# Optimization experiments

Measured on AMD Instinct MI355X. Metric: run time of the kernel, lower is better.

## Reference

```python
import jax, jax.numpy as jnp
import numpy as np

D = 128  # node_dim (hardcoded in the torch module)


def _bn(x, g, b, eps=1e-5):
    # BatchNorm1d in training mode: per-batch mean / biased variance
    m = x.mean(0)
    v = x.var(0)
    return (x - m) * jax.lax.rsqrt(v + eps) * g + b


def setup_inputs() -> dict:
    key = jax.random.key(0)
    ks = jax.random.split(key, 16)
    N, E, ED = 4096, 16384, 16
    node = jax.random.normal(ks[0], (N, D), jnp.float32)
    edge = jax.random.normal(ks[1], (E, ED), jnp.float32)
    hidden = jax.random.normal(ks[2], (1, N, D), jnp.float32)
    edge_index = jax.random.randint(ks[3], (E, 2), 0, N)

    def lin(k, o, i):
        return jax.random.normal(k, (o, i), jnp.float32) / np.sqrt(i).astype(np.float32)

    W1 = lin(ks[4], 256, ED)
    W2 = lin(ks[5], 256, 256)
    W3 = lin(ks[6], 128, 256)
    W4 = lin(ks[7], D * D, 128)
    g1, b1 = jnp.ones(256), jnp.zeros(256)
    g2, b2 = jnp.ones(256), jnp.zeros(256)
    g3, b3 = jnp.ones(128), jnp.zeros(128)
    g4, b4 = jnp.ones(D * D), jnp.zeros(D * D)
    lim = 1.0 / np.sqrt(D).astype(np.float32)
    bias = jax.random.uniform(ks[8], (D,), jnp.float32, -lim, lim)
    W_ih = lin(ks[9], 3 * D, D)
    W_hh = lin(ks[10], 3 * D, D)
    b_ih = jnp.zeros(3 * D)
    b_hh = jnp.zeros(3 * D)
    return dict(node=node, edge_index=edge_index, edge=edge, hidden=hidden,
                W1=W1, g1=g1, b1=b1, W2=W2, g2=g2, b2=b2, W3=W3, g3=g3, b3=b3,
                W4=W4, g4=g4, b4=b4, bias=bias, W_ih=W_ih, W_hh=W_hh,
                b_ih=b_ih, b_hh=b_hh)


def reference(node, edge_index, edge, hidden, W1, g1, b1, W2, g2, b2,
              W3, g3, b3, W4, g4, b4, bias, W_ih, W_hh, b_ih, b_hh):
    N = node.shape[0]
    E = edge.shape[0]
    h0 = hidden[0]  # [N, D]
    src, dst = edge_index[:, 0], edge_index[:, 1]

    # edge encoder -> per-edge [D, D] weight matrix
    x = jax.nn.relu(_bn(edge @ W1.T, g1, b1))
    x = jax.nn.relu(_bn(x @ W2.T, g2, b2))
    x = jax.nn.relu(_bn(x @ W3.T, g3, b3))
    w = _bn(x @ W4.T, g4, b4).reshape(E, D, D)

    # gather source nodes, per-edge vector-matrix product
    x_i = node[src]                               # [E, D]
    msg = jnp.einsum('ed,edk->ek', x_i, w)        # [E, D]

    # scatter-mean over destination nodes
    sums = jax.ops.segment_sum(msg, dst, num_segments=N)
    cnt = jax.ops.segment_sum(jnp.ones((E, 1), msg.dtype), dst, num_segments=N)
    message = sums / jnp.maximum(cnt, 1.0)
    m = jax.nn.relu(message + bias)               # [N, D]

    # single-step GRU (PyTorch gate order r, z, n)
    gi = m @ W_ih.T + b_ih
    gh = h0 @ W_hh.T + b_hh
    r = jax.nn.sigmoid(gi[:, :D] + gh[:, :D])
    z = jax.nn.sigmoid(gi[:, D:2 * D] + gh[:, D:2 * D])
    n = jnp.tanh(gi[:, 2 * D:] + r * gh[:, 2 * D:])
    hn = (1.0 - z) * n + z * h0                   # [N, D]
    return hn, hn[None]
```

## Files before the change

### kernel.cpp

```cpp
#include <hip/hip_runtime.h>

#define EPS 1e-5f

typedef _Float16 half8 __attribute__((ext_vector_type(8)));
typedef _Float16 half4 __attribute__((ext_vector_type(4)));
typedef float f32x16 __attribute__((ext_vector_type(16)));

__global__ __launch_bounds__(256) void gemm_abt(const float* __restrict__ A,
                                                const float* __restrict__ B,
                                                _Float16* __restrict__ C,
                                                int M, int N, int K,
                                                float* __restrict__ osum,
                                                float* __restrict__ osq) {
  __shared__ float As[16][68];
  __shared__ float Bs[16][68];
  const int t = threadIdx.x;
  const int tx = t & 15, ty = t >> 4;
  const int m0 = blockIdx.y * 64, n0 = blockIdx.x * 64;
  float acc[4][4] = {};
  for (int k0 = 0; k0 < K; k0 += 16) {
    __syncthreads();
    {
      const int r = t >> 2;
      const int kk = (t & 3) << 2;
      float4 av = *(const float4*)&A[(size_t)(m0 + r) * K + k0 + kk];
      As[kk + 0][r] = av.x; As[kk + 1][r] = av.y;
      As[kk + 2][r] = av.z; As[kk + 3][r] = av.w;
      float4 bv = *(const float4*)&B[(size_t)(n0 + r) * K + k0 + kk];
      Bs[kk + 0][r] = bv.x; Bs[kk + 1][r] = bv.y;
      Bs[kk + 2][r] = bv.z; Bs[kk + 3][r] = bv.w;
    }
    __syncthreads();
#pragma unroll
    for (int kk = 0; kk < 16; ++kk) {
      float4 a = *(const float4*)&As[kk][ty << 2];
      float4 b = *(const float4*)&Bs[kk][tx << 2];
      float av[4] = {a.x, a.y, a.z, a.w};
      float bv[4] = {b.x, b.y, b.z, b.w};
#pragma unroll
      for (int i = 0; i < 4; ++i)
#pragma unroll
        for (int j = 0; j < 4; ++j) acc[i][j] += av[i] * bv[j];
    }
  }
#pragma unroll
  for (int i = 0; i < 4; ++i) {
    half4 o;
    o[0] = (_Float16)acc[i][0]; o[1] = (_Float16)acc[i][1];
    o[2] = (_Float16)acc[i][2]; o[3] = (_Float16)acc[i][3];
    *(half4*)&C[(size_t)(m0 + (ty << 2) + i) * N + n0 + (tx << 2)] = o;
  }
  __syncthreads();
  float* sred = (float*)As;
  if (t < 128) sred[t] = 0.f;
  __syncthreads();
#pragma unroll
  for (int j = 0; j < 4; ++j) {
    float s = 0.f, sq = 0.f;
#pragma unroll
    for (int i = 0; i < 4; ++i) {
      float v = acc[i][j];
      s += v; sq += v * v;
    }
    atomicAdd(&sred[((tx << 2) + j) * 2 + 0], s);
    atomicAdd(&sred[((tx << 2) + j) * 2 + 1], sq);
  }
  __syncthreads();
  if (t < 64) {
    atomicAdd(&osum[n0 + t], sred[t * 2]);
    atomicAdd(&osq[n0 + t], sred[t * 2 + 1]);
  }
}

template <int TRANS, bool STATS, bool AH, bool CH>
__global__ __launch_bounds__(256) void gemm16(const void* __restrict__ Ap,
                                              const float* __restrict__ B,
                                              void* __restrict__ Cp,
                                              int lda, int ldb, int ldc, int K,
                                              const float* __restrict__ s1,
                                              const float* __restrict__ s2,
                                              const float* __restrict__ g,
                                              const float* __restrict__ b,
                                              float invM,
                                              float* __restrict__ osum,
                                              float* __restrict__ osq) {
  __shared__ _Float16 As[128 * 64];
  __shared__ _Float16 Bs[128 * 64];
  __shared__ float scL[256], shL[256];
  const int t = threadIdx.x;
  const int m0 = blockIdx.y * 128, n0 = blockIdx.x * 128;
  const int w = t >> 6, l = t & 63;
  const int wm = w >> 1, wn = w & 1;
  const int lr = l & 31, lg = l >> 5;
  if (TRANS == 1) {
    if (t < K) {
      float mean = s1[t] * invM;
      float var = s2[t] * invM - mean * mean;
      float sc = g[t] * rsqrtf(var + EPS);
      scL[t] = sc;
      shL[t] = b[t] - mean * sc;
    }
  }
  f32x16 acc[2][2];
#pragma unroll
  for (int i = 0; i < 2; ++i)
#pragma unroll
    for (int j = 0; j < 2; ++j) acc[i][j] = (f32x16){0.f};
  for (int k0 = 0; k0 < K; k0 += 64) {
    __syncthreads();
#pragma unroll
    for (int i = 0; i < 4; ++i) {
      const int gq = i * 256 + t;
      const int f = gq >> 6, lp = gq & 63;
      const int row = (f >> 2) * 32 + (lp & 31);
      const int c = (f & 3) * 16 + (lp >> 5) * 8;
      float va[8];
      if (AH) {
        const _Float16* ap = (const _Float16*)Ap + (size_t)(m0 + row) * lda + k0 + c;
        half8 av = *(const half8*)ap;
#pragma unroll
        for (int j = 0; j < 8; ++j) va[j] = (float)av[j];
      } else {
        const float* ap = (const float*)Ap + (size_t)(m0 + row) * lda + k0 + c;
        float4 a4 = *(const float4*)ap, b4 = *(const float4*)(ap + 4);
        va[0] = a4.x; va[1] = a4.y; va[2] = a4.z; va[3] = a4.w;
        va[4] = b4.x; va[5] = b4.y; va[6] = b4.z; va[7] = b4.w;
      }
      if (TRANS == 1) {
#pragma unroll
        for (int j = 0; j < 8; ++j)
          va[j] = fmaxf(va[j] * scL[k0 + c + j] + shL[k0 + c + j], 0.f);
      }
      half8 h;
#pragma unroll
      for (int j = 0; j < 8; ++j) h[j] = (_Float16)va[j];
      *(half8*)(As + (size_t)gq * 8) = h;
      const float* bp = B + (size_t)(n0 + row) * ldb + k0 + c;
      float4 e4 = *(const float4*)bp, f4 = *(const float4*)(bp + 4);
      half8 hb;
      hb[0] = (_Float16)e4.x; hb[1] = (_Float16)e4.y; hb[2] = (_Float16)e4.z; hb[3] = (_Float16)e4.w;
      hb[4] = (_Float16)f4.x; hb[5] = (_Float16)f4.y; hb[6] = (_Float16)f4.z; hb[7] = (_Float16)f4.w;
      *(half8*)(Bs + (size_t)gq * 8) = hb;
    }
    __syncthreads();
#pragma unroll
    for (int ks = 0; ks < 4; ++ks) {
      half8 af[2], bf[2];
#pragma unroll
      for (int mb = 0; mb < 2; ++mb) {
        af[mb] = *(const half8*)(As + (size_t)(((wm * 2 + mb) * 4 + ks) * 64 + l) * 8);
        bf[mb] = *(const half8*)(Bs + (size_t)(((wn * 2 + mb) * 4 + ks) * 64 + l) * 8);
      }
#pragma unroll
      for (int mb = 0; mb < 2; ++mb)
#pragma unroll
        for (int nb = 0; nb < 2; ++nb)
          acc[mb][nb] = __builtin_amdgcn_mfma_f32_32x32x16_f16(af[mb], bf[nb], acc[mb][nb], 0, 0, 0);
    }
  }
#pragma unroll
  for (int mb = 0; mb < 2; ++mb)
#pragma unroll
    for (int nb = 0; nb < 2; ++nb)
#pragma unroll
      for (int r = 0; r < 16; ++r) {
        const int row = m0 + wm * 64 + mb * 32 + (r & 3) + 8 * (r >> 2) + 4 * lg;
        const int col = n0 + wn * 64 + nb * 32 + lr;
        if (CH) ((_Float16*)Cp)[(size_t)row * ldc + col] = (_Float16)acc[mb][nb][r];
        else ((float*)Cp)[(size_t)row * ldc + col] = acc[mb][nb][r];
      }
  if (STATS) {
    __syncthreads();
    float* sred = (float*)As;
    if (t < 256) sred[t] = 0.f;
    __syncthreads();
#pragma unroll
    for (int nb = 0; nb < 2; ++nb) {
      float s = 0.f, sq = 0.f;
#pragma unroll
      for (int mb = 0; mb < 2; ++mb)
#pragma unroll
        for (int r = 0; r < 16; ++r) {
          float v = acc[mb][nb][r];
          s += v; sq += v * v;
        }
      const int cl = wn * 64 + nb * 32 + lr;
      atomicAdd(&sred[cl * 2 + 0], s);
      atomicAdd(&sred[cl * 2 + 1], sq);
    }
    __syncthreads();
    if (t < 128) {
      atomicAdd(&osum[n0 + t], sred[t * 2]);
      atomicAdd(&osq[n0 + t], sred[t * 2 + 1]);
    }
  }
}

__global__ __launch_bounds__(256) void gram_kernel(const _Float16* __restrict__ y3,
                                                   float* __restrict__ part,
                                                   const float* __restrict__ s3sum,
                                                   const float* __restrict__ s3sq,
                                                   const float* __restrict__ g3,
                                                   const float* __restrict__ b3,
                                                   float invE,
                                                   float* __restrict__ colsum) {
  __shared__ float xL[128 * 132];
  __shared__ float scL[128], shL[128];
  const int t = threadIdx.x, tx = t & 15, ty = t >> 4;
  if (t < 128) {
    float mean = s3sum[t] * invE;
    float var = s3sq[t] * invE - mean * mean;
    float sc = g3[t] * rsqrtf(var + EPS);
    scL[t] = sc;
    shL[t] = b3[t] - mean * sc;
  }
  __syncthreads();
  const int r0 = blockIdx.x * 128;
#pragma unroll
  for (int i = 0; i < 16; ++i) {
    int f4 = t + i * 256;
    int r = f4 >> 5;
    int c4 = (f4 & 31) << 2;
    half4 hv = *(const half4*)&y3[(size_t)(r0 + r) * 128 + c4];
    float4 v;
    v.x = fmaxf((float)hv[0] * scL[c4 + 0] + shL[c4 + 0], 0.f);
    v.y = fmaxf((float)hv[1] * scL[c4 + 1] + shL[c4 + 1], 0.f);
    v.z = fmaxf((float)hv[2] * scL[c4 + 2] + shL[c4 + 2], 0.f);
    v.w = fmaxf((float)hv[3] * scL[c4 + 3] + shL[c4 + 3], 0.f);
    *(float4*)&xL[r * 132 + c4] = v;
  }
  __syncthreads();
  float acc[8][8] = {};
  float csum[8] = {};
  for (int r = 0; r < 128; ++r) {
    float4 a0 = *(const float4*)&xL[r * 132 + ty * 8];
    float4 a1 = *(const float4*)&xL[r * 132 + ty * 8 + 4];
    float4 b0 = *(const float4*)&xL[r * 132 + tx * 8];
    float4 b1 = *(const float4*)&xL[r * 132 + tx * 8 + 4];
    float a[8] = {a0.x, a0.y, a0.z, a0.w, a1.x, a1.y, a1.z, a1.w};
    float b[8] = {b0.x, b0.y, b0.z, b0.w, b1.x, b1.y, b1.z, b1.w};
#pragma unroll
    for (int i = 0; i < 8; ++i)
#pragma unroll
      for (int j = 0; j < 8; ++j) acc[i][j] += a[i] * b[j];
    if (tx == ty) {
#pragma unroll
      for (int i = 0; i < 8; ++i) csum[i] += a[i];
    }
  }
  float* base = part + (size_t)blockIdx.x * 16384;
#pragma unroll
  for (int i = 0; i < 8; ++i)
#pragma unroll
    for (int j = 0; j < 8; ++j)
      base[(ty * 8 + i) * 128 + tx * 8 + j] = acc[i][j];
  if (tx == ty) {
#pragma unroll
    for (int i = 0; i < 8; ++i) atomicAdd(&colsum[ty * 8 + i], csum[i]);
  }
}

__global__ __launch_bounds__(256) void gram_reduce(const float* __restrict__ part,
                                                   float* __restrict__ out) {
  int idx = blockIdx.x * 256 + threadIdx.x;
  float s = 0.f;
  for (int b = 0; b < 128; ++b) s += part[(size_t)b * 16384 + idx];
  out[idx] = s;
}

__global__ __launch_bounds__(256) void w4_finalize(const float* __restrict__ W4,
                                                   const float* __restrict__ U,
                                                   const float* __restrict__ colsum3,
                                                   const float* __restrict__ g4,
                                                   const float* __restrict__ b4,
                                                   _Float16* __restrict__ BTf,
                                                   float* __restrict__ t4,
                                                   float invM) {
  const int r = (blockIdx.x * 256 + threadIdx.x) >> 6;
  const int lane = threadIdx.x & 63;
  const float* wp = W4 + (size_t)r * 128;
  const float* up = U + (size_t)r * 128;
  float p1 = 0.f, p2 = 0.f;
#pragma unroll
  for (int c0 = 0; c0 < 128; c0 += 64) {
    float wv = wp[c0 + lane];
    p1 += up[c0 + lane] * wv;
    p2 += colsum3[c0 + lane] * wv;
  }
#pragma unroll
  for (int off = 32; off > 0; off >>= 1) {
    p1 += __shfl_down(p1, off);
    p2 += __shfl_down(p2, off);
  }
  p1 = __shfl(p1, 0);
  p2 = __shfl(p2, 0);
  float m4 = p2 * invM;
  float q = p1 * invM;
  float s = g4[r] * rsqrtf(q - m4 * m4 + EPS);
  if (lane == 0) t4[r] = b4[r] - m4 * s;
  const int kout = r & 127, d = r >> 7;
  if (lane < 16) {
    const int ks = lane >> 1, lg = lane & 1;
    const float* cp = wp + lane * 8;
    float4 va = *(const float4*)cp, vb = *(const float4*)(cp + 4);
    half8 h;
    h[0] = (_Float16)(s * va.x); h[1] = (_Float16)(s * va.y);
    h[2] = (_Float16)(s * va.z); h[3] = (_Float16)(s * va.w);
    h[4] = (_Float16)(s * vb.x); h[5] = (_Float16)(s * vb.y);
    h[6] = (_Float16)(s * vb.z); h[7] = (_Float16)(s * vb.w);
    size_t off16 = (size_t)d * 16384 +
                   (size_t)((((kout >> 5) * 8 + ks) * 64) + (kout & 31) + lg * 32) * 8;
    *(half8*)(BTf + off16) = h;
  }
}

__global__ __launch_bounds__(256, 2) void zgemm(const _Float16* __restrict__ y3,
                                                const float* __restrict__ node,
                                                const int* __restrict__ eidx,
                                                const _Float16* __restrict__ BTf,
                                                const float* __restrict__ Tn,
                                                const float* __restrict__ s3sum,
                                                const float* __restrict__ s3sq,
                                                const float* __restrict__ g3,
                                                const float* __restrict__ b3,
                                                float invE,
                                                float* __restrict__ sums) {
  __shared__ __align__(16) _Float16 Bs[2][16384];
  __shared__ _Float16 xiL[32 * 128];
  __shared__ float scL[128], shL[128];
  const int t = threadIdx.x;
  const int e0 = blockIdx.y * 128;
  const int d0 = blockIdx.x * 32;
  const int w = t >> 6, l = t & 63;
  const int wm = w >> 1, wn = w & 1;
  const int lr = l & 31, lg = l >> 5;
  if (t < 128) {
    float mean = s3sum[t] * invE;
    float var = s3sq[t] * invE - mean * mean;
    float sc = g3[t] * rsqrtf(var + EPS);
    scL[t] = sc;
    shL[t] = b3[t] - mean * sc;
  }
  {
    const int e = t >> 1, db = (t & 1) * 16;
    const int src = eidx[(e0 + e) * 2];
    const float* np = node + (size_t)src * 128 + d0 + db;
#pragma unroll
    for (int j = 0; j < 16; j += 4) {
      float4 v = *(const float4*)(np + j);
      xiL[(db + j + 0) * 128 + e] = (_Float16)v.x;
      xiL[(db + j + 1) * 128 + e] = (_Float16)v.y;
      xiL[(db + j + 2) * 128 + e] = (_Float16)v.z;
      xiL[(db + j + 3) * 128 + e] = (_Float16)v.w;
    }
  }
  half8 st[8];
  {
    const _Float16* p = BTf + (size_t)d0 * 16384 + (size_t)t * 8;
#pragma unroll
    for (int j = 0; j < 8; ++j) st[j] = *(const half8*)(p + j * 2048);
  }
#pragma unroll
  for (int j = 0; j < 8; ++j) *(half8*)(&Bs[0][0] + t * 8 + j * 2048) = st[j];
  {
    const _Float16* p = BTf + (size_t)(d0 + 1) * 16384 + (size_t)t * 8;
#pragma unroll
    for (int j = 0; j < 8; ++j) st[j] = *(const half8*)(p + j * 2048);
  }
  __syncthreads();
  half8 xf[2][8];
#pragma unroll
  for (int mb = 0; mb < 2; ++mb) {
    const _Float16* xp = y3 + (size_t)(e0 + wm * 64 + mb * 32 + lr) * 128 + lg * 8;
#pragma unroll
    for (int ks = 0; ks < 8; ++ks) {
      const int c = ks * 16 + lg * 8;
      half8 hv = *(const half8*)(xp + ks * 16);
      half8 h;
#pragma unroll
      for (int j = 0; j < 8; ++j)
        h[j] = (_Float16)fmaxf((float)hv[j] * scL[c + j] + shL[c + j], 0.f);
      xf[mb][ks] = h;
    }
  }
  f32x16 acc00 = (f32x16){0.f}, acc01 = (f32x16){0.f};
  f32x16 acc10 = (f32x16){0.f}, acc11 = (f32x16){0.f};

  for (int dt = 0; dt < 32; ++dt) {
    const _Float16* bs = &Bs[dt & 1][0];
    _Float16* bsn = &Bs[(dt + 1) & 1][0];
    const _Float16 xv0 = xiL[dt * 128 + wm * 64 + lr];
    const _Float16 xv1 = xiL[dt * 128 + wm * 64 + 32 + lr];
    const half8 xb0 = {xv0, xv0, xv0, xv0, xv0, xv0, xv0, xv0};
    const half8 xb1 = {xv1, xv1, xv1, xv1, xv1, xv1, xv1, xv1};
    __builtin_amdgcn_s_setprio(1);
#pragma unroll
    for (int ks = 0; ks < 8; ++ks) {
      half8 b0 = *(const half8*)(bs + (size_t)(((wn * 2 + 0) * 8 + ks) * 64 + l) * 8);
      half8 b1 = *(const half8*)(bs + (size_t)(((wn * 2 + 1) * 8 + ks) * 64 + l) * 8);
      if (dt < 31) *(half8*)(bsn + t * 8 + ks * 2048) = st[ks];
      half8 a0 = xf[0][ks] * xb0;
      half8 a1 = xf[1][ks] * xb1;
      acc00 = __builtin_amdgcn_mfma_f32_32x32x16_f16(a0, b0, acc00, 0, 0, 0);
      acc01 = __builtin_amdgcn_mfma_f32_32x32x16_f16(a0, b1, acc01, 0, 0, 0);
      acc10 = __builtin_amdgcn_mfma_f32_32x32x16_f16(a1, b0, acc10, 0, 0, 0);
      acc11 = __builtin_amdgcn_mfma_f32_32x32x16_f16(a1, b1, acc11, 0, 0, 0);
    }
    __builtin_amdgcn_s_setprio(0);
    if (dt < 30) {
      const _Float16* p = BTf + (size_t)(d0 + dt + 2) * 16384 + (size_t)t * 8;
#pragma unroll
      for (int j = 0; j < 8; ++j) st[j] = *(const half8*)(p + j * 2048);
    }
    asm volatile("s_waitcnt lgkmcnt(0)" ::: "memory");
    __builtin_amdgcn_s_barrier();
  }
  const bool add_t = (blockIdx.x == 0);
#pragma unroll
  for (int r = 0; r < 16; ++r) {
    const int rl = (r & 3) + 8 * (r >> 2) + 4 * lg;
    const int eA = e0 + wm * 64 + rl;
    const int eB = eA + 32;
    const int dA = eidx[eA * 2 + 1], sA = eidx[eA * 2];
    const int dB = eidx[eB * 2 + 1], sB = eidx[eB * 2];
    const int c0 = wn * 64 + lr;
    float v00 = acc00[r], v01 = acc01[r], v10 = acc10[r], v11 = acc11[r];
    if (add_t) {
      v00 += Tn[(size_t)sA * 128 + c0];
      v01 += Tn[(size_t)sA * 128 + c0 + 32];
      v10 += Tn[(size_t)sB * 128 + c0];
      v11 += Tn[(size_t)sB * 128 + c0 + 32];
    }
    atomicAdd(&sums[(size_t)dA * 128 + c0], v00);
    atomicAdd(&sums[(size_t)dA * 128 + c0 + 32], v01);
    atomicAdd(&sums[(size_t)dB * 128 + c0], v10);
    atomicAdd(&sums[(size_t)dB * 128 + c0 + 32], v11);
  }
}

__global__ __launch_bounds__(128) void t4n_kernel(const float* __restrict__ node,
                                                  const float* __restrict__ t4,
                                                  float* __restrict__ Tn,
                                                  const int* __restrict__ eidx,
                                                  float* __restrict__ cnt, int E) {
  __shared__ float nodeL[8][128];
  const int k = threadIdx.x;
  const int n0 = blockIdx.x * 8;
  {
    int e = blockIdx.x * 32 + k;
    if (k < 32 && e < E) atomicAdd(&cnt[eidx[e * 2 + 1]], 1.0f);
  }
#pragma unroll
  for (int j = 0; j < 8; ++j) nodeL[j][k] = node[(size_t)(n0 + j) * 128 + k];
  __syncthreads();
  float acc[8] = {};
  for (int d = 0; d < 128; ++d) {
    float wv = t4[d * 128 + k];
#pragma unroll
    for (int j = 0; j < 8; ++j) acc[j] += nodeL[j][d] * wv;
  }
#pragma unroll
  for (int j = 0; j < 8; ++j) Tn[(size_t)(n0 + j) * 128 + k] = acc[j];
}

__global__ __launch_bounds__(256) void gru_gates(const float* __restrict__ sums,
                                                 const float* __restrict__ cnt,
                                                 const float* __restrict__ bias,
                                                 const float* __restrict__ h0,
                                                 const float* __restrict__ Wih,
                                                 const float* __restrict__ Whh,
                                                 float* __restrict__ gi,
                                                 float* __restrict__ gh) {
  __shared__ _Float16 As[128 * 64];
  __shared__ _Float16 Bs[128 * 64];
  const bool isgh = blockIdx.x >= 3;
  const float* A = isgh ? h0 : sums;
  const float* B = isgh ? Whh : Wih;
  float* C = isgh ? gh : gi;
  const int n0 = (isgh ? blockIdx.x - 3 : blockIdx.x) * 128;
  const int m0 = blockIdx.y * 128;
  const int t = threadIdx.x;
  const int w = t >> 6, l = t & 63;
  const int wm = w >> 1, wn = w & 1;
  const int lr = l & 31, lg = l >> 5;
  f32x16 acc[2][2];
#pragma unroll
  for (int i = 0; i < 2; ++i)
#pragma unroll
    for (int j = 0; j < 2; ++j) acc[i][j] = (f32x16){0.f};
  for (int k0 = 0; k0 < 128; k0 += 64) {
    __syncthreads();
#pragma unroll
    for (int i = 0; i < 4; ++i) {
      const int gq = i * 256 + t;
      const int f = gq >> 6, lp = gq & 63;
      const int row = (f >> 2) * 32 + (lp & 31);
      const int c = (f & 3) * 16 + (lp >> 5) * 8;
      const float* ap = A + (size_t)(m0 + row) * 128 + k0 + c;
      float4 a4 = *(const float4*)ap, b4 = *(const float4*)(ap + 4);
      float va[8] = {a4.x, a4.y, a4.z, a4.w, b4.x, b4.y, b4.z, b4.w};
      if (!isgh) {
        float rc = 1.f / fmaxf(cnt[m0 + row], 1.f);
#pragma unroll
        for (int j = 0; j < 8; ++j) va[j] = fmaxf(va[j] * rc + bias[k0 + c + j], 0.f);
      }
      half8 h;
#pragma unroll
      for (int j = 0; j < 8; ++j) h[j] = (_Float16)va[j];
      *(half8*)(As + (size_t)gq * 8) = h;
      const float* bp = B + (size_t)(n0 + row) * 128 + k0 + c;
      float4 e4 = *(const float4*)bp, f4 = *(const float4*)(bp + 4);
      half8 hb;
      hb[0] = (_Float16)e4.x; hb[1] = (_Float16)e4.y; hb[2] = (_Float16)e4.z; hb[3] = (_Float16)e4.w;
      hb[4] = (_Float16)f4.x; hb[5] = (_Float16)f4.y; hb[6] = (_Float16)f4.z; hb[7] = (_Float16)f4.w;
      *(half8*)(Bs + (size_t)gq * 8) = hb;
    }
    __syncthreads();
#pragma unroll
    for (int ks = 0; ks < 4; ++ks) {
      half8 af[2], bf[2];
#pragma unroll
      for (int mb = 0; mb < 2; ++mb) {
        af[mb] = *(const half8*)(As + (size_t)(((wm * 2 + mb) * 4 + ks) * 64 + l) * 8);
        bf[mb] = *(const half8*)(Bs + (size_t)(((wn * 2 + mb) * 4 + ks) * 64 + l) * 8);
      }
#pragma unroll
      for (int mb = 0; mb < 2; ++mb)
#pragma unroll
        for (int nb = 0; nb < 2; ++nb)
          acc[mb][nb] = __builtin_amdgcn_mfma_f32_32x32x16_f16(af[mb], bf[nb], acc[mb][nb], 0, 0, 0);
    }
  }
#pragma unroll
  for (int mb = 0; mb < 2; ++mb)
#pragma unroll
    for (int nb = 0; nb < 2; ++nb)
#pragma unroll
      for (int r = 0; r < 16; ++r) {
        const int row = m0 + wm * 64 + mb * 32 + (r & 3) + 8 * (r >> 2) + 4 * lg;
        const int col = n0 + wn * 64 + nb * 32 + lr;
        C[(size_t)row * 384 + col] = acc[mb][nb][r];
      }
}

__global__ __launch_bounds__(256) void gru_finalize(const float* __restrict__ gi,
                                                    const float* __restrict__ gh,
                                                    const float* __restrict__ h0,
                                                    const float* __restrict__ bih,
                                                    const float* __restrict__ bhh,
                                                    float* __restrict__ out, int Nn) {
  int idx = blockIdx.x * 256 + threadIdx.x;
  int n = idx >> 7, k = idx & 127;
  const float* gin = gi + (size_t)n * 384;
  const float* ghn = gh + (size_t)n * 384;
  float r = 1.f / (1.f + expf(-(gin[k] + bih[k] + ghn[k] + bhh[k])));
  float z = 1.f / (1.f + expf(-(gin[128 + k] + bih[128 + k] + ghn[128 + k] + bhh[128 + k])));
  float nn = tanhf(gin[256 + k] + bih[256 + k] + r * (ghn[256 + k] + bhh[256 + k]));
  float h = h0[idx];
  float hn = (1.f - z) * nn + z * h;
  out[idx] = hn;
  out[idx + (size_t)Nn * 128] = hn;
}

extern "C" void kernel_launch(void* const* d_in, const int* in_sizes, int n_in,
                              void* d_out, int out_size, void* d_ws, size_t ws_size,
                              hipStream_t stream) {
  const float* node = (const float*)d_in[0];
  const int* eidx = (const int*)d_in[1];
  const float* edge = (const float*)d_in[2];
  const float* hidden = (const float*)d_in[3];
  const float* W1 = (const float*)d_in[4];
  const float* g1 = (const float*)d_in[5];
  const float* b1 = (const float*)d_in[6];
  const float* W2 = (const float*)d_in[7];
  const float* g2 = (const float*)d_in[8];
  const float* b2 = (const float*)d_in[9];
  const float* W3 = (const float*)d_in[10];
  const float* g3 = (const float*)d_in[11];
  const float* b3 = (const float*)d_in[12];
  const float* W4 = (const float*)d_in[13];
  const float* g4 = (const float*)d_in[14];
  const float* b4 = (const float*)d_in[15];
  const float* bias = (const float*)d_in[16];
  const float* Wih = (const float*)d_in[17];
  const float* Whh = (const float*)d_in[18];
  const float* bih = (const float*)d_in[19];
  const float* bhh = (const float*)d_in[20];
  float* out = (float*)d_out;

  const int Nn = in_sizes[0] / 128;
  const int E = in_sizes[2] / 16;
  const float invE = 1.0f / (float)E;

  float* ws = (float*)d_ws;
  _Float16* y1h = (_Float16*)(ws + 0);
  float* gpart = ws + 0;
  float* ybuf2 = ws + 4194304;
  _Float16* y2h = (_Float16*)ybuf2;
  _Float16* y3h = (_Float16*)(ws + 8388608);
  _Float16* BTf = (_Float16*)(ws + 10485760);
  float* t4 = ws + 11534336;
  float* stats = ws + 11550720;
  float* G3 = ws + 11552512;
  float* sums = ws + 11568896;
  float* cnt = ws + 12093184;
  float* Tn = ws + 12097280;
  float* stat1 = stats, *stat2 = stats + 512, *stat3 = stats + 1024;
  float* colsum3 = stats + 1536;
  float* U = ybuf2;
  float* gi = ybuf2;
  float* gh = ybuf2 + 1572864;

  hipMemsetAsync(stats, 0, 1664 * sizeof(float), stream);
  hipMemsetAsync(sums, 0, ((size_t)Nn * 128 + Nn) * sizeof(float), stream);

  gemm_abt<<<dim3(4, E / 64), 256, 0, stream>>>(edge, W1, y1h, E, 256, 16, stat1, stat1 + 256);
  gemm16<1, true, true, true><<<dim3(2, E / 128), 256, 0, stream>>>(
      y1h, W2, y2h, 256, 256, 256, 256, stat1, stat1 + 256, g1, b1, invE, stat2, stat2 + 256);
  gemm16<1, true, true, true><<<dim3(1, E / 128), 256, 0, stream>>>(
      y2h, W3, y3h, 256, 256, 128, 256, stat2, stat2 + 256, g2, b2, invE, stat3, stat3 + 256);

  gram_kernel<<<E / 128, 256, 0, stream>>>(y3h, gpart, stat3, stat3 + 256, g3, b3, invE,
                                           colsum3);
  gram_reduce<<<64, 256, 0, stream>>>(gpart, G3);

  gemm16<0, false, false, false><<<dim3(1, 16384 / 128), 256, 0, stream>>>(
      W4, G3, U, 128, 128, 128, 128, nullptr, nullptr, nullptr, nullptr, 0.f, nullptr, nullptr);
  w4_finalize<<<16384 / 4, 256, 0, stream>>>(W4, U, colsum3, g4, b4, BTf, t4, invE);
  t4n_kernel<<<Nn / 8, 128, 0, stream>>>(node, t4, Tn, eidx, cnt, E);

  zgemm<<<dim3(4, E / 128), 256, 0, stream>>>(y3h, node, eidx, BTf, Tn,
                                              stat3, stat3 + 256, g3, b3, invE, sums);

  gru_gates<<<dim3(6, Nn / 128), 256, 0, stream>>>(sums, cnt, bias, hidden, Wih, Whh, gi, gh);
  gru_finalize<<<Nn * 128 / 256, 256, 0, stream>>>(gi, gh, hidden, bih, bhh, out, Nn);
}
```

Before: 239.9 us.

## Load B fragments directly from global memory instead of LDS double buffering

The zgemm kernel no longer stages the per-dt B tile through a double-buffered 64 KB LDS array with register prefetch and barriers. Each wave now loads its own MFMA B fragments straight from global memory (through L2/L1) at the start of every dt iteration. This removes the LDS traffic, the per-iteration barrier and most of the LDS footprint, which may allow more blocks per CU. In exchange there is no explicit prefetch: global load latency is exposed each iteration unless other waves hide it, and the two waves that share a wn column both fetch the same B data.

```diff
diff --git a/kernel.cpp b/kernel.cpp
--- a/kernel.cpp
+++ b/kernel.cpp
@@ -325,7 +325,6 @@
                                                 const float* __restrict__ b3,
                                                 float invE,
                                                 float* __restrict__ sums) {
-  __shared__ __align__(16) _Float16 Bs[2][16384];
   __shared__ _Float16 xiL[32 * 128];
   __shared__ float scL[128], shL[128];
   const int t = threadIdx.x;
@@ -354,19 +353,6 @@
       xiL[(db + j + 3) * 128 + e] = (_Float16)v.w;
     }
   }
-  half8 st[8];
-  {
-    const _Float16* p = BTf + (size_t)d0 * 16384 + (size_t)t * 8;
-#pragma unroll
-    for (int j = 0; j < 8; ++j) st[j] = *(const half8*)(p + j * 2048);
-  }
-#pragma unroll
-  for (int j = 0; j < 8; ++j) *(half8*)(&Bs[0][0] + t * 8 + j * 2048) = st[j];
-  {
-    const _Float16* p = BTf + (size_t)(d0 + 1) * 16384 + (size_t)t * 8;
-#pragma unroll
-    for (int j = 0; j < 8; ++j) st[j] = *(const half8*)(p + j * 2048);
-  }
   __syncthreads();
   half8 xf[2][8];
 #pragma unroll
@@ -386,34 +372,29 @@
   f32x16 acc00 = (f32x16){0.f}, acc01 = (f32x16){0.f};
   f32x16 acc10 = (f32x16){0.f}, acc11 = (f32x16){0.f};
 
+  const _Float16* b0base = BTf + ((size_t)((wn * 2 + 0) * 8) * 64 + l) * 8;
+  const _Float16* b1base = BTf + ((size_t)((wn * 2 + 1) * 8) * 64 + l) * 8;
   for (int dt = 0; dt < 32; ++dt) {
-    const _Float16* bs = &Bs[dt & 1][0];
-    _Float16* bsn = &Bs[(dt + 1) & 1][0];
+    const size_t toff = (size_t)(d0 + dt) * 16384;
+    half8 bf0[8], bf1[8];
+#pragma unroll
+    for (int ks = 0; ks < 8; ++ks) {
+      bf0[ks] = *(const half8*)(b0base + toff + ks * 512);
+      bf1[ks] = *(const half8*)(b1base + toff + ks * 512);
+    }
     const _Float16 xv0 = xiL[dt * 128 + wm * 64 + lr];
     const _Float16 xv1 = xiL[dt * 128 + wm * 64 + 32 + lr];
     const half8 xb0 = {xv0, xv0, xv0, xv0, xv0, xv0, xv0, xv0};
     const half8 xb1 = {xv1, xv1, xv1, xv1, xv1, xv1, xv1, xv1};
-    __builtin_amdgcn_s_setprio(1);
 #pragma unroll
     for (int ks = 0; ks < 8; ++ks) {
-      half8 b0 = *(const half8*)(bs + (size_t)(((wn * 2 + 0) * 8 + ks) * 64 + l) * 8);
-      half8 b1 = *(const half8*)(bs + (size_t)(((wn * 2 + 1) * 8 + ks) * 64 + l) * 8);
-      if (dt < 31) *(half8*)(bsn + t * 8 + ks * 2048) = st[ks];
       half8 a0 = xf[0][ks] * xb0;
       half8 a1 = xf[1][ks] * xb1;
-      acc00 = __builtin_amdgcn_mfma_f32_32x32x16_f16(a0, b0, acc00, 0, 0, 0);
-      acc01 = __builtin_amdgcn_mfma_f32_32x32x16_f16(a0, b1, acc01, 0, 0, 0);
-      acc10 = __builtin_amdgcn_mfma_f32_32x32x16_f16(a1, b0, acc10, 0, 0, 0);
-      acc11 = __builtin_amdgcn_mfma_f32_32x32x16_f16(a1, b1, acc11, 0, 0, 0);
-    }
-    __builtin_amdgcn_s_setprio(0);
-    if (dt < 30) {
-      const _Float16* p = BTf + (size_t)(d0 + dt + 2) * 16384 + (size_t)t * 8;
-#pragma unroll
-      for (int j = 0; j < 8; ++j) st[j] = *(const half8*)(p + j * 2048);
-    }
-    asm volatile("s_waitcnt lgkmcnt(0)" ::: "memory");
-    __builtin_amdgcn_s_barrier();
+      acc00 = __builtin_amdgcn_mfma_f32_32x32x16_f16(a0, bf0[ks], acc00, 0, 0, 0);
+      acc01 = __builtin_amdgcn_mfma_f32_32x32x16_f16(a0, bf1[ks], acc01, 0, 0, 0);
+      acc10 = __builtin_amdgcn_mfma_f32_32x32x16_f16(a1, bf0[ks], acc10, 0, 0, 0);
+      acc11 = __builtin_amdgcn_mfma_f32_32x32x16_f16(a1, bf1[ks], acc11, 0, 0, 0);
+    }
   }
   const bool add_t = (blockIdx.x == 0);
 #pragma unroll
```

Measured after the change: 269.4 us. 1.12x slower.
